# Performance work log

Measured on AMD Instinct MI355X. Metric: run time of the kernel, lower is better.

## Reference

```python
import jax, jax.numpy as jnp
import numpy as np

B, SD, AD, H, QE, NQ = 16384, 512, 64, 1024, 64, 64


def setup_inputs() -> dict:
    key = jax.random.key(0)
    ks = jax.random.split(key, 12)
    s = 0.02
    p = lambda k, shape: (jax.random.normal(k, shape, jnp.float32) * s)
    return {
        "state": jax.random.normal(ks[0], (B, SD), jnp.float32),
        "action": jax.random.normal(ks[1], (B, AD), jnp.float32),
        # twin critics: leading axis 2 stacks q1 / q2 parameters
        "W_e1": p(ks[2], (2, QE, 1)),      "b_e1": p(ks[3], (2, QE)),
        "W_e2": p(ks[4], (2, QE, QE)),     "b_e2": p(ks[5], (2, QE)),
        "W_f1": p(ks[6], (2, H, SD + AD)), "b_f1": p(ks[7], (2, H)),
        "g1": jnp.ones((2, H), jnp.float32),  "beta1": jnp.zeros((2, H), jnp.float32),
        "W_f2": p(ks[8], (2, H, H)),       "b_f2": p(ks[9], (2, H)),
        "g2": jnp.ones((2, H), jnp.float32),  "beta2": jnp.zeros((2, H), jnp.float32),
        "W_h": p(ks[10], (2, 1, H + QE)),  "b_h": p(ks[11], (2, 1)),
    }


def _layernorm(x, g, b, eps=1e-5):
    mu = x.mean(-1, keepdims=True)
    var = ((x - mu) ** 2).mean(-1, keepdims=True)
    return (x - mu) * jax.lax.rsqrt(var + eps) * g + b


def _qnet(state, action, W_e1, b_e1, W_e2, b_e2, W_f1, b_f1, g1, beta1,
          W_f2, b_f2, g2, beta2, W_h, b_h):
    # feature_net (eval mode: dropout is identity)
    x = jnp.concatenate([state, action], axis=-1)            # [B, SD+AD]
    h = jax.nn.relu(_layernorm(x @ W_f1.T + b_f1, g1, beta1))
    feat = jax.nn.relu(_layernorm(h @ W_f2.T + b_f2, g2, beta2))  # [B, H]
    # tau embedding (batch-independent -> compute once per quantile, not per sample)
    tau = (jnp.linspace(0.0, 1.0, NQ + 1)[:-1] + 1.0 / (2 * NQ))[:, None]  # [NQ,1]
    te = jax.nn.relu(tau @ W_e1.T + b_e1) @ W_e2.T + b_e2    # [NQ, QE]
    # head on concat([feat, te]) == linear split (exact same math as the 64-iter loop)
    q_feat = feat @ W_h[0, :H]                               # [B]
    q_tau = te @ W_h[0, H:]                                  # [NQ]
    return q_feat[:, None] + q_tau[None, :] + b_h[0]         # [B, NQ]


def reference(state, action, W_e1, b_e1, W_e2, b_e2, W_f1, b_f1, g1, beta1,
              W_f2, b_f2, g2, beta2, W_h, b_h):
    qnet = lambda *ps: _qnet(state, action, *ps)
    q = jax.vmap(qnet)(W_e1, b_e1, W_e2, b_e2, W_f1, b_f1, g1, beta1,
                       W_f2, b_f2, g2, beta2, W_h, b_h)      # [2, B, NQ]
    return q[0], q[1]
```

## Files before the change

### kernel.cpp

```cpp
#include <hip/hip_runtime.h>
#include <stdint.h>

#define BATCH 16384
#define SDIM 512
#define ADIM 64
#define XDIM 576
#define HDIM 1024
#define NQD 64
#define QED 64

typedef __attribute__((ext_vector_type(8))) short short8;
typedef __attribute__((ext_vector_type(4))) float f32x4;

static __device__ inline unsigned short f2bf(float f) {
  unsigned int u = __float_as_uint(f);
  unsigned int r = (u + 0x7fffu + ((u >> 16) & 1u)) >> 16;
  return (unsigned short)r;
}
static __device__ inline float bf2f(unsigned short u) {
  return __uint_as_float(((unsigned int)u) << 16);
}

static __device__ inline void gload_lds16(const void* g, void* l) {
  __builtin_amdgcn_global_load_lds(
      (const __attribute__((address_space(1))) uint32_t*)g,
      (__attribute__((address_space(3))) uint32_t*)l, 16, 0, 0);
}


__global__ __launch_bounds__(256) void prep(const float* __restrict__ st,
                                            const float* __restrict__ ac,
                                            unsigned short* __restrict__ xb,
                                            const float* __restrict__ w1s,
                                            unsigned short* __restrict__ w1d,
                                            const float* __restrict__ w2s,
                                            unsigned short* __restrict__ w2d) {
  const int nx = BATCH * XDIM / 4;
  const int n1 = 2 * HDIM * XDIM / 4;
  const int n2 = 2 * HDIM * HDIM / 4;
  for (int i = blockIdx.x * blockDim.x + threadIdx.x; i < nx + n1 + n2;
       i += gridDim.x * blockDim.x) {
    float4 v;
    unsigned short* dst;
    int di;
    if (i < nx) {
      const int e = i * 4;
      const int b = e / XDIM;
      const int j = e - b * XDIM;
      if (j < SDIM) v = *(const float4*)(st + (size_t)b * SDIM + j);
      else          v = *(const float4*)(ac + (size_t)b * ADIM + (j - SDIM));
      dst = xb; di = i;
    } else if (i < nx + n1) {
      di = i - nx; v = ((const float4*)w1s)[di]; dst = w1d;
    } else {
      di = i - nx - n1; v = ((const float4*)w2s)[di]; dst = w2d;
    }
    ushort4 o;
    o.x = f2bf(v.x); o.y = f2bf(v.y); o.z = f2bf(v.z); o.w = f2bf(v.w);
    ((ushort4*)dst)[di] = o;
  }
}


__global__ void qtau_kernel(const float* __restrict__ We1, const float* __restrict__ be1,
                            const float* __restrict__ We2, const float* __restrict__ be2,
                            const float* __restrict__ Wh,  const float* __restrict__ bh,
                            float* __restrict__ qtau) {
  const int c = blockIdx.x >> 6;
  const int nq = blockIdx.x & 63;
  const int q = threadIdx.x;
  const float tau = (float)nq / 64.0f + 0.0078125f;
  float acc = be2[c * 64 + q];
  for (int e = 0; e < 64; ++e) {
    const float t1 = fmaxf(tau * We1[c * 64 + e] + be1[c * 64 + e], 0.0f);
    acc += t1 * We2[(c * 64 + q) * 64 + e];
  }
  float v = acc * Wh[c * (HDIM + QED) + HDIM + q];
  #pragma unroll
  for (int off = 32; off; off >>= 1) v += __shfl_xor(v, off);
  if (q == 0) qtau[c * 64 + nq] = v + bh[c];
}


template <int K>
__global__ __launch_bounds__(512, 4) void gemm_bc(const unsigned short* __restrict__ Abase,
                                                  size_t aCritStride,
                                                  const unsigned short* __restrict__ Wbase,
                                                  const float* __restrict__ biasBase,
                                                  unsigned short* __restrict__ Cbase) {
  constexpr int NT = K / 32;
  __shared__ unsigned short As[2][256][32];
  __shared__ unsigned short Bs[2][128][32];

  const int tid  = threadIdx.x;
  const int lane = tid & 63;
  const int wave = tid >> 6;
  const int wm = wave >> 1;
  const int wn = wave & 1;

  const int bid = (int)blockIdx.x;
  const int L = (bid & 7) * 128 + (bid >> 3);
  const int n = L & 7;
  const int cidx = (L >> 3) & 1;
  const int m = L >> 4;
  const int mBase = m * 256;
  const int nBase = n * 128;

  const unsigned short* A = Abase + aCritStride * (size_t)cidx;
  const unsigned short* W = Wbase + (size_t)cidx * HDIM * K;
  const float* bias = biasBase + cidx * HDIM;
  unsigned short* C = Cbase + (size_t)cidx * BATCH * HDIM;

  auto stage = [&](int buf, int kt) {
    #pragma unroll
    for (int i = 0; i < 2; ++i) {
      const int flat = i * 512 + tid;
      const int row  = flat >> 2;
      const int ls   = (flat & 3) ^ ((row >> 1) & 3);
      gload_lds16(A + (size_t)(mBase + row) * K + kt * 32 + ls * 8,
                  &As[buf][0][0] + (size_t)flat * 8);
    }
    {
      const int row = tid >> 2;
      const int ls  = (tid & 3) ^ ((row >> 1) & 3);
      gload_lds16(W + (size_t)(nBase + row) * K + kt * 32 + ls * 8,
                  &Bs[buf][0][0] + (size_t)tid * 8);
    }
  };

  f32x4 acc[4][4];
  #pragma unroll
  for (int fm = 0; fm < 4; ++fm)
    #pragma unroll
    for (int fn = 0; fn < 4; ++fn) {
      f32x4 z = {0.f, 0.f, 0.f, 0.f};
      acc[fm][fn] = z;
    }

  stage(0, 0);
  __syncthreads();

  for (int t = 0; t < NT; ++t) {
    const int buf = t & 1;
    if (t + 1 < NT) stage(buf ^ 1, t + 1);

    short8 af[4], bf[4];
    #pragma unroll
    for (int fm = 0; fm < 4; ++fm) {
      const int r  = wm * 64 + fm * 16 + (lane & 15);
      const int ps = (lane >> 4) ^ ((r >> 1) & 3);
      af[fm] = *(const short8*)&As[buf][r][ps * 8];
    }
    #pragma unroll
    for (int fn = 0; fn < 4; ++fn) {
      const int r  = wn * 64 + fn * 16 + (lane & 15);
      const int ps = (lane >> 4) ^ ((r >> 1) & 3);
      bf[fn] = *(const short8*)&Bs[buf][r][ps * 8];
    }

    __builtin_amdgcn_s_setprio(1);
    #pragma unroll
    for (int fm = 0; fm < 4; ++fm)
      #pragma unroll
      for (int fn = 0; fn < 4; ++fn)
        acc[fm][fn] = __builtin_amdgcn_mfma_f32_16x16x32_bf16(af[fm], bf[fn],
                                                              acc[fm][fn], 0, 0, 0);
    __builtin_amdgcn_s_setprio(0);
    __syncthreads();
  }

  __syncthreads();
  unsigned short* patch = ((unsigned short*)&As[0][0][0]) + wave * 2304;

  float bcol[4];
  #pragma unroll
  for (int fn = 0; fn < 4; ++fn)
    bcol[fn] = bias[nBase + wn * 64 + fn * 16 + (lane & 15)];

  const int cBase = nBase + wn * 64;

  #pragma unroll
  for (int p = 0; p < 2; ++p) {
    #pragma unroll
    for (int f2 = 0; f2 < 2; ++f2) {
      const int fm = p * 2 + f2;
      #pragma unroll
      for (int fn = 0; fn < 4; ++fn) {
        const int rl = f2 * 16 + (lane >> 4) * 4;
        const int cl = fn * 16 + (lane & 15);
        #pragma unroll
        for (int j = 0; j < 4; ++j)
          patch[(rl + j) * 72 + cl] = f2bf(acc[fm][fn][j] + bcol[fn]);
      }
    }
    #pragma unroll
    for (int k = 0; k < 4; ++k) {
      const int rl = k * 8 + (lane >> 3);
      const short8 v = *(const short8*)&patch[rl * 72 + (lane & 7) * 8];
      const int rowg = mBase + wm * 64 + p * 32 + rl;
      *(short8*)(C + (size_t)rowg * HDIM + cBase + (lane & 7) * 8) = v;
    }
  }
}


template <bool HEAD>
__global__ __launch_bounds__(256) void ln_bc(const unsigned short* __restrict__ Xb,
                                             const float* __restrict__ gB,
                                             const float* __restrict__ btB,
                                             unsigned short* __restrict__ Yb,
                                             const float* __restrict__ WhB,
                                             const float* __restrict__ qtB,
                                             float* __restrict__ outB) {
  const int gb = blockIdx.x;
  const int c = gb >> 14;
  const int row = gb & (BATCH - 1);
  const unsigned short* X = Xb + ((size_t)c * BATCH + row) * HDIM;
  const float* g   = gB + c * HDIM;
  const float* bta = btB + c * HDIM;

  const int tid = threadIdx.x;
  const int lane = tid & 63;
  const int wave = tid >> 6;
  __shared__ float rs_[4], rq_[4], rp_[4];

  const ushort4 xv = ((const ushort4*)X)[tid];
  const float x0 = bf2f(xv.x), x1 = bf2f(xv.y), x2 = bf2f(xv.z), x3 = bf2f(xv.w);
  float s = x0 + x1 + x2 + x3;
  float q = x0 * x0 + x1 * x1 + x2 * x2 + x3 * x3;
  #pragma unroll
  for (int off = 32; off; off >>= 1) {
    s += __shfl_xor(s, off);
    q += __shfl_xor(q, off);
  }
  if (lane == 0) { rs_[wave] = s; rq_[wave] = q; }
  __syncthreads();
  s = rs_[0] + rs_[1] + rs_[2] + rs_[3];
  q = rq_[0] + rq_[1] + rq_[2] + rq_[3];
  const float mu = s * (1.0f / 1024.0f);
  const float var = q * (1.0f / 1024.0f) - mu * mu;
  const float rsig = rsqrtf(var + 1e-5f);

  const float4 gv = ((const float4*)g)[tid];
  const float4 bv = ((const float4*)bta)[tid];
  const float y0 = fmaxf((x0 - mu) * rsig * gv.x + bv.x, 0.0f);
  const float y1 = fmaxf((x1 - mu) * rsig * gv.y + bv.y, 0.0f);
  const float y2 = fmaxf((x2 - mu) * rsig * gv.z + bv.z, 0.0f);
  const float y3 = fmaxf((x3 - mu) * rsig * gv.w + bv.w, 0.0f);

  if constexpr (!HEAD) {
    ushort4 o;
    o.x = f2bf(y0); o.y = f2bf(y1); o.z = f2bf(y2); o.w = f2bf(y3);
    ((ushort4*)(Yb + ((size_t)c * BATCH + row) * HDIM))[tid] = o;
  } else {
    const float* Wh = WhB + c * (HDIM + QED);
    const float4 wv = ((const float4*)Wh)[tid];
    float p = y0 * wv.x + y1 * wv.y + y2 * wv.z + y3 * wv.w;
    #pragma unroll
    for (int off = 32; off; off >>= 1) p += __shfl_xor(p, off);
    if (lane == 0) rp_[wave] = p;
    __syncthreads();
    if (tid < 64) {
      const float qf = rp_[0] + rp_[1] + rp_[2] + rp_[3];
      outB[((size_t)c * BATCH + row) * NQD + tid] = qf + qtB[c * 64 + tid];
    }
  }
}


extern "C" void kernel_launch(void* const* d_in, const int* in_sizes, int n_in,
                              void* d_out, int out_size, void* d_ws, size_t ws_size,
                              hipStream_t stream) {
  (void)in_sizes; (void)n_in; (void)out_size; (void)ws_size;
  const float* state  = (const float*)d_in[0];
  const float* action = (const float*)d_in[1];
  const float* We1 = (const float*)d_in[2];
  const float* be1 = (const float*)d_in[3];
  const float* We2 = (const float*)d_in[4];
  const float* be2 = (const float*)d_in[5];
  const float* Wf1 = (const float*)d_in[6];
  const float* bW1 = (const float*)d_in[7];
  const float* g1  = (const float*)d_in[8];
  const float* bt1 = (const float*)d_in[9];
  const float* Wf2 = (const float*)d_in[10];
  const float* bW2 = (const float*)d_in[11];
  const float* g2  = (const float*)d_in[12];
  const float* bt2 = (const float*)d_in[13];
  const float* Wh  = (const float*)d_in[14];
  const float* bh  = (const float*)d_in[15];
  float* out = (float*)d_out;

  char* ws = (char*)d_ws;
  unsigned short* xb   = (unsigned short*)(ws);
  unsigned short* w1b  = (unsigned short*)(ws + 18874368);
  unsigned short* w2b  = (unsigned short*)(ws + 21233664);
  float*          qtw  = (float*)(ws + 25427968);
  unsigned short* ha   = (unsigned short*)(ws + 25428480);
  unsigned short* hb   = (unsigned short*)(ws + 92537344);

  prep<<<2048, 256, 0, stream>>>(state, action, xb, Wf1, w1b, Wf2, w2b);
  qtau_kernel<<<128, 64, 0, stream>>>(We1, be1, We2, be2, Wh, bh, qtw);

  gemm_bc<XDIM><<<1024, 512, 0, stream>>>(xb, 0, w1b, bW1, ha);
  ln_bc<false><<<2 * BATCH, 256, 0, stream>>>(ha, g1, bt1, hb, nullptr, nullptr, nullptr);
  gemm_bc<HDIM><<<1024, 512, 0, stream>>>(hb, (size_t)BATCH * HDIM, w2b, bW2, ha);
  ln_bc<true><<<2 * BATCH, 256, 0, stream>>>(ha, g2, bt2, nullptr, Wh, qtw, out);
}
```

Measured before the change: 198.2 us.

## Fuse first LayerNorm into GEMM epilogue stats and second GEMM A-load

Removes the standalone LayerNorm+ReLU pass after the first GEMM. The first GEMM now emits per-row partial sums and sums of squares from its epilogue, a small kernel reduces them into mean and rsigma, and the second GEMM applies normalize, affine and ReLU to A fragments as it reads them from LDS before the MFMAs. This drops one full bf16 activation write and read, at the cost of extra ALU work inside the second GEMM's inner loop and scratch stats kept in the output buffer before it is overwritten.

```diff
diff --git a/kernel.cpp b/kernel.cpp
--- a/kernel.cpp
+++ b/kernel.cpp
@@ -82,12 +82,32 @@
 }
 
 
-template <int K>
+__global__ __launch_bounds__(256) void stats_reduce(const float2* __restrict__ pstat,
+                                                    float2* __restrict__ musig) {
+  const int i = blockIdx.x * 256 + threadIdx.x;
+  float s = 0.f, q = 0.f;
+  #pragma unroll
+  for (int k = 0; k < 16; ++k) {
+    const float2 v = pstat[(size_t)i * 16 + k];
+    s += v.x; q += v.y;
+  }
+  const float mu = s * (1.0f / 1024.0f);
+  const float var = q * (1.0f / 1024.0f) - mu * mu;
+  float2 o; o.x = mu; o.y = rsqrtf(var + 1e-5f);
+  musig[i] = o;
+}
+
+
+template <int K, bool STATS, bool XFORM>
 __global__ __launch_bounds__(512, 4) void gemm_bc(const unsigned short* __restrict__ Abase,
                                                   size_t aCritStride,
                                                   const unsigned short* __restrict__ Wbase,
                                                   const float* __restrict__ biasBase,
-                                                  unsigned short* __restrict__ Cbase) {
+                                                  unsigned short* __restrict__ Cbase,
+                                                  const float2* __restrict__ musigB,
+                                                  const float* __restrict__ gB,
+                                                  const float* __restrict__ bB,
+                                                  float2* __restrict__ pstat) {
   constexpr int NT = K / 32;
   __shared__ unsigned short As[2][256][32];
   __shared__ unsigned short Bs[2][128][32];
@@ -110,6 +130,9 @@
   const unsigned short* W = Wbase + (size_t)cidx * HDIM * K;
   const float* bias = biasBase + cidx * HDIM;
   unsigned short* C = Cbase + (size_t)cidx * BATCH * HDIM;
+  const float2* musig = XFORM ? (musigB + (size_t)cidx * BATCH) : nullptr;
+  const float* gv = XFORM ? (gB + cidx * HDIM) : nullptr;
+  const float* bv = XFORM ? (bB + cidx * HDIM) : nullptr;
 
   auto stage = [&](int buf, int kt) {
     #pragma unroll
@@ -145,11 +168,41 @@
     if (t + 1 < NT) stage(buf ^ 1, t + 1);
 
     short8 af[4], bf[4];
-    #pragma unroll
-    for (int fm = 0; fm < 4; ++fm) {
-      const int r  = wm * 64 + fm * 16 + (lane & 15);
-      const int ps = (lane >> 4) ^ ((r >> 1) & 3);
-      af[fm] = *(const short8*)&As[buf][r][ps * 8];
+    if constexpr (XFORM) {
+      const int k0 = t * 32 + (lane >> 4) * 8;
+      const float4 g0 = *(const float4*)(gv + k0);
+      const float4 g1 = *(const float4*)(gv + k0 + 4);
+      const float4 b0 = *(const float4*)(bv + k0);
+      const float4 b1 = *(const float4*)(bv + k0 + 4);
+      const float gk[8] = {g0.x, g0.y, g0.z, g0.w, g1.x, g1.y, g1.z, g1.w};
+      const float bk[8] = {b0.x, b0.y, b0.z, b0.w, b1.x, b1.y, b1.z, b1.w};
+      #pragma unroll
+      for (int fm = 0; fm < 4; ++fm) {
+        const int r  = wm * 64 + fm * 16 + (lane & 15);
+        const int ps = (lane >> 4) ^ ((r >> 1) & 3);
+        union { short8 s; unsigned int u[4]; } rd, cv;
+        rd.s = *(const short8*)&As[buf][r][ps * 8];
+        const float2 ms = musig[mBase + r];
+        const float rsf = ms.y;
+        const float nmu = -ms.x * rsf;
+        #pragma unroll
+        for (int d = 0; d < 4; ++d) {
+          const unsigned int w = rd.u[d];
+          const float xlo = __uint_as_float(w << 16);
+          const float xhi = __uint_as_float(w & 0xffff0000u);
+          const float ylo = fmaxf(fmaf(fmaf(xlo, rsf, nmu), gk[2 * d],     bk[2 * d]),     0.f);
+          const float yhi = fmaxf(fmaf(fmaf(xhi, rsf, nmu), gk[2 * d + 1], bk[2 * d + 1]), 0.f);
+          asm("v_cvt_pk_bf16_f32 %0, %1, %2" : "=v"(cv.u[d]) : "v"(ylo), "v"(yhi));
+        }
+        af[fm] = cv.s;
+      }
+    } else {
+      #pragma unroll
+      for (int fm = 0; fm < 4; ++fm) {
+        const int r  = wm * 64 + fm * 16 + (lane & 15);
+        const int ps = (lane >> 4) ^ ((r >> 1) & 3);
+        af[fm] = *(const short8*)&As[buf][r][ps * 8];
+      }
     }
     #pragma unroll
     for (int fn = 0; fn < 4; ++fn) {
@@ -179,6 +232,12 @@
 
   const int cBase = nBase + wn * 64;
 
+  float sA[16], qA[16];
+  if constexpr (STATS) {
+    #pragma unroll
+    for (int i = 0; i < 16; ++i) { sA[i] = 0.f; qA[i] = 0.f; }
+  }
+
   #pragma unroll
   for (int p = 0; p < 2; ++p) {
     #pragma unroll
@@ -189,8 +248,15 @@
         const int rl = f2 * 16 + (lane >> 4) * 4;
         const int cl = fn * 16 + (lane & 15);
         #pragma unroll
-        for (int j = 0; j < 4; ++j)
-          patch[(rl + j) * 72 + cl] = f2bf(acc[fm][fn][j] + bcol[fn]);
+        for (int j = 0; j < 4; ++j) {
+          const unsigned short o = f2bf(acc[fm][fn][j] + bcol[fn]);
+          patch[(rl + j) * 72 + cl] = o;
+          if constexpr (STATS) {
+            const float vb = bf2f(o);
+            sA[fm * 4 + j] += vb;
+            qA[fm * 4 + j] += vb * vb;
+          }
+        }
       }
     }
     #pragma unroll
@@ -201,17 +267,35 @@
       *(short8*)(C + (size_t)rowg * HDIM + cBase + (lane & 7) * 8) = v;
     }
   }
-}
-
-
-template <bool HEAD>
-__global__ __launch_bounds__(256) void ln_bc(const unsigned short* __restrict__ Xb,
-                                             const float* __restrict__ gB,
-                                             const float* __restrict__ btB,
-                                             unsigned short* __restrict__ Yb,
-                                             const float* __restrict__ WhB,
-                                             const float* __restrict__ qtB,
-                                             float* __restrict__ outB) {
+
+  if constexpr (STATS) {
+    #pragma unroll
+    for (int off = 1; off < 16; off <<= 1)
+      #pragma unroll
+      for (int i = 0; i < 16; ++i) {
+        sA[i] += __shfl_xor(sA[i], off);
+        qA[i] += __shfl_xor(qA[i], off);
+      }
+    if ((lane & 15) == 0) {
+      const int slot = n * 2 + wn;
+      #pragma unroll
+      for (int i = 0; i < 16; ++i) {
+        const int p = i >> 3, f2 = (i >> 2) & 1, j = i & 3;
+        const int row = mBase + wm * 64 + p * 32 + f2 * 16 + (lane >> 4) * 4 + j;
+        float2 o; o.x = sA[i]; o.y = qA[i];
+        pstat[((size_t)cidx * BATCH + row) * 16 + slot] = o;
+      }
+    }
+  }
+}
+
+
+__global__ __launch_bounds__(256) void ln_head_bc(const unsigned short* __restrict__ Xb,
+                                                  const float* __restrict__ gB,
+                                                  const float* __restrict__ btB,
+                                                  const float* __restrict__ WhB,
+                                                  const float* __restrict__ qtB,
+                                                  float* __restrict__ outB) {
   const int gb = blockIdx.x;
   const int c = gb >> 14;
   const int row = gb & (BATCH - 1);
@@ -248,22 +332,16 @@
   const float y2 = fmaxf((x2 - mu) * rsig * gv.z + bv.z, 0.0f);
   const float y3 = fmaxf((x3 - mu) * rsig * gv.w + bv.w, 0.0f);
 
-  if constexpr (!HEAD) {
-    ushort4 o;
-    o.x = f2bf(y0); o.y = f2bf(y1); o.z = f2bf(y2); o.w = f2bf(y3);
-    ((ushort4*)(Yb + ((size_t)c * BATCH + row) * HDIM))[tid] = o;
-  } else {
-    const float* Wh = WhB + c * (HDIM + QED);
-    const float4 wv = ((const float4*)Wh)[tid];
-    float p = y0 * wv.x + y1 * wv.y + y2 * wv.z + y3 * wv.w;
-    #pragma unroll
-    for (int off = 32; off; off >>= 1) p += __shfl_xor(p, off);
-    if (lane == 0) rp_[wave] = p;
-    __syncthreads();
-    if (tid < 64) {
-      const float qf = rp_[0] + rp_[1] + rp_[2] + rp_[3];
-      outB[((size_t)c * BATCH + row) * NQD + tid] = qf + qtB[c * 64 + tid];
-    }
+  const float* Wh = WhB + c * (HDIM + QED);
+  const float4 wv = ((const float4*)Wh)[tid];
+  float p = y0 * wv.x + y1 * wv.y + y2 * wv.z + y3 * wv.w;
+  #pragma unroll
+  for (int off = 32; off; off >>= 1) p += __shfl_xor(p, off);
+  if (lane == 0) rp_[wave] = p;
+  __syncthreads();
+  if (tid < 64) {
+    const float qf = rp_[0] + rp_[1] + rp_[2] + rp_[3];
+    outB[((size_t)c * BATCH + row) * NQD + tid] = qf + qtB[c * 64 + tid];
   }
 }
 
@@ -298,11 +376,16 @@
   unsigned short* ha   = (unsigned short*)(ws + 25428480);
   unsigned short* hb   = (unsigned short*)(ws + 92537344);
 
+  float2* pstat = (float2*)out;
+  float2* musig = (float2*)(out + 2 * BATCH * 16 * 2);
+
   prep<<<2048, 256, 0, stream>>>(state, action, xb, Wf1, w1b, Wf2, w2b);
   qtau_kernel<<<128, 64, 0, stream>>>(We1, be1, We2, be2, Wh, bh, qtw);
 
-  gemm_bc<XDIM><<<1024, 512, 0, stream>>>(xb, 0, w1b, bW1, ha);
-  ln_bc<false><<<2 * BATCH, 256, 0, stream>>>(ha, g1, bt1, hb, nullptr, nullptr, nullptr);
-  gemm_bc<HDIM><<<1024, 512, 0, stream>>>(hb, (size_t)BATCH * HDIM, w2b, bW2, ha);
-  ln_bc<true><<<2 * BATCH, 256, 0, stream>>>(ha, g2, bt2, nullptr, Wh, qtw, out);
-}
+  gemm_bc<XDIM, true, false><<<1024, 512, 0, stream>>>(
+      xb, 0, w1b, bW1, ha, nullptr, nullptr, nullptr, pstat);
+  stats_reduce<<<128, 256, 0, stream>>>(pstat, musig);
+  gemm_bc<HDIM, false, true><<<1024, 512, 0, stream>>>(
+      ha, (size_t)BATCH * HDIM, w2b, bW2, hb, musig, g1, bt1, nullptr);
+  ln_head_bc<<<2 * BATCH, 256, 0, stream>>>(hb, g2, bt2, Wh, qtw, out);
+}
```

Result: slower. 233.8 us (+17.9%).
